# Kernel optimization log

Hardware: AMD Instinct MI355X
Metric: run time of the kernel (lower is better)

Reference implementation:

```python
import jax, jax.numpy as jnp
import numpy as np

BN_EPS = 1e-5


def cond_conv(x, att_w, att_b, weight, pad):
    """CondConv: per-sample expert-mixed conv.
    x: [N,C,H,W]; att_w: [K,C]; att_b: [K]; weight: [K,O,I,kh,kw]; pad: (ph,pw)."""
    pooled = x.mean(axis=(2, 3))                         # [N,C]  (AdaptiveAvgPool2d(1))
    att = jax.nn.sigmoid(pooled @ att_w.T + att_b)       # [N,K]  (1x1 conv + sigmoid)
    agg_w = jnp.einsum('nk,koihw->noihw', att, weight)   # per-sample kernels [N,O,I,kh,kw]

    def conv1(xi, wi):
        return jax.lax.conv_general_dilated(
            xi[None], wi, window_strides=(1, 1),
            padding=[(pad[0], pad[0]), (pad[1], pad[1])],
            dimension_numbers=('NCHW', 'OIHW', 'NCHW'))[0]

    return jax.vmap(conv1)(x, agg_w)                     # [N,O,H,W]


def batchnorm(x, gamma, beta):
    # training-mode BN: biased batch stats over (N,H,W)
    mean = x.mean(axis=(0, 2, 3), keepdims=True)
    var = x.var(axis=(0, 2, 3), keepdims=True)
    xn = (x - mean) * jax.lax.rsqrt(var + BN_EPS)
    return xn * gamma[None, :, None, None] + beta[None, :, None, None]


def channel_shuffle(x, g):
    N, C, H, W = x.shape
    return x.reshape(N, g, C // g, H, W).transpose(0, 2, 1, 3, 4).reshape(N, C, H, W)


def setup_inputs() -> dict:
    key = jax.random.key(0)
    ks = jax.random.split(key, 8)
    N, C, H, W = 32, 256, 64, 64
    Cb, K = C // 4, 4
    inp = {
        'x': jax.random.normal(ks[0], (N, C, H, W), jnp.float32),
        'sq_att_w': jax.random.normal(ks[1], (K, Cb), jnp.float32) * 0.1,
        'sq_att_b': jnp.zeros((K,), jnp.float32),
        'sq_w': jax.random.normal(ks[2], (K, Cb, Cb, 3, 3), jnp.float32) * 0.05,
        'sq_g': jnp.ones((Cb,), jnp.float32),
        'sq_b': jnp.zeros((Cb,), jnp.float32),
        'ver_att_w': jax.random.normal(ks[3], (K, Cb), jnp.float32) * 0.1,
        'ver_att_b': jnp.zeros((K,), jnp.float32),
        'ver_w': jax.random.normal(ks[4], (K, Cb, Cb, 3, 1), jnp.float32) * 0.05,
        'ver_g': jnp.ones((Cb,), jnp.float32),
        'ver_b': jnp.zeros((Cb,), jnp.float32),
        'hor_att_w': jax.random.normal(ks[5], (K, Cb), jnp.float32) * 0.1,
        'hor_att_b': jnp.zeros((K,), jnp.float32),
        'hor_w': jax.random.normal(ks[6], (K, Cb, Cb, 1, 3), jnp.float32) * 0.05,
        'hor_g': jnp.ones((Cb,), jnp.float32),
        'hor_b': jnp.zeros((Cb,), jnp.float32),
    }
    return inp


def reference(x, sq_att_w, sq_att_b, sq_w, sq_g, sq_b,
              ver_att_w, ver_att_b, ver_w, ver_g, ver_b,
              hor_att_w, hor_att_b, hor_w, hor_g, hor_b):
    # q_Split: chunk into 4 along channels
    s0, s1, s2, s3 = jnp.split(x, 4, axis=1)
    # square branch: CondConv 3x3 pad 1 + BN
    sq = batchnorm(cond_conv(s1, sq_att_w, sq_att_b, sq_w, (1, 1)), sq_g, sq_b)
    # vertical branch: CondConv 3x1 pad (1,0) + BN (crop layer is Identity since offset=0)
    ve = batchnorm(cond_conv(s2, ver_att_w, ver_att_b, ver_w, (1, 0)), ver_g, ver_b)
    # horizontal branch: CondConv 1x3 pad (0,1) + BN
    ho = batchnorm(cond_conv(s3, hor_att_w, hor_att_b, hor_w, (0, 1)), hor_g, hor_b)
    out = jnp.concatenate((s0, sq, ve, ho), axis=1)
    return channel_shuffle(out, 8)
```

## Files before the change

kernel.cpp:

```cpp
#include <hip/hip_runtime.h>
#include <cstddef>
#include <cstdint>


typedef __attribute__((ext_vector_type(8))) short frag8;
typedef __attribute__((ext_vector_type(16))) float accf16;

#define HW 4096
#define CNT_INV (1.0f / 131072.0f)
#define CSTR 1056
#define RSTR 8448
#define XT_BR (32ull * 66 * 8448)

#define WS_POOLED 0
#define WS_SS     24576
#define WS_PST    24960
#define WS_WBF_SQ  221568
#define WS_WBF_VER 811392
#define WS_WBF_HOR 1008000
#define WS_XT      1204608
#define WS_CVOUT   14586240

__device__ __forceinline__ int shuf_ch(int c) { return ((c & 31) << 3) | (c >> 5); }

__device__ __forceinline__ unsigned bf16pair(float a, float b) {
    unsigned ua = __builtin_bit_cast(unsigned, a);
    unsigned ub = __builtin_bit_cast(unsigned, b);
    ua = (ua + 0x7fffu + ((ua >> 16) & 1u)) >> 16;
    ub = (ub + 0x7fffu + ((ub >> 16) & 1u)) >> 16;
    return ua | (ub << 16);
}

__device__ __forceinline__ unsigned short bf16r(float a) {
    unsigned ua = __builtin_bit_cast(unsigned, a);
    return (unsigned short)((ua + 0x7fffu + ((ua >> 16) & 1u)) >> 16);
}

__device__ __forceinline__ float bf16lo(unsigned u) {
    return __builtin_bit_cast(float, u << 16);
}
__device__ __forceinline__ float bf16hi(unsigned u) {
    return __builtin_bit_cast(float, u & 0xffff0000u);
}

__device__ __forceinline__ void gload_lds16(const void* g, void* l) {
    __builtin_amdgcn_global_load_lds(
        (const __attribute__((address_space(1))) void*)g,
        (__attribute__((address_space(3))) void*)l, 16, 0, 0);
}

__global__ void __launch_bounds__(256) prepass_kernel(
    const float* __restrict__ x, unsigned char* __restrict__ xt,
    float* __restrict__ pooled4) {
    const int bid = blockIdx.x;
    const int hq = bid & 3;
    const int c8 = (bid >> 2) & 7;
    const int n = (bid >> 5) & 31;
    const int b = bid >> 10;
    const int tid = threadIdx.x;
    const int w = tid & 63, q = tid >> 6;
    const float* xb = x + (size_t)(n * 256 + 64 * (b + 1) + c8 * 8) * HW;
    unsigned char* xtb = xt + (size_t)b * XT_BR + (size_t)n * 66 * RSTR + c8 * CSTR;

    float ps[8] = {0.f, 0.f, 0.f, 0.f, 0.f, 0.f, 0.f, 0.f};
#pragma unroll
    for (int it = 0; it < 4; ++it) {
        const int h = hq * 16 + it * 4 + q;
        float v[8];
#pragma unroll
        for (int j = 0; j < 8; ++j) v[j] = xb[(size_t)j * HW + h * 64 + w];
        unsigned pk[4];
#pragma unroll
        for (int j = 0; j < 4; ++j) pk[j] = bf16pair(v[2 * j], v[2 * j + 1]);
        *(uint4*)(xtb + (size_t)(h + 1) * RSTR + (w + 1) * 16) = *(uint4*)pk;
#pragma unroll
        for (int j = 0; j < 8; ++j) ps[j] += v[j];
    }
    if (hq == 0) {
        for (int idx = tid; idx < 260; idx += 256) {
            int p, slot;
            if (idx < 66)       { p = 0;         slot = idx; }
            else if (idx < 132) { p = 65;        slot = idx - 66; }
            else if (idx < 196) { p = idx - 131; slot = 0; }
            else                { p = idx - 195; slot = 65; }
            *(uint4*)(xtb + (size_t)p * RSTR + slot * 16) = uint4{0, 0, 0, 0};
        }
    }
    __shared__ float red[4][8];
#pragma unroll
    for (int j = 0; j < 8; ++j)
#pragma unroll
        for (int off = 32; off; off >>= 1) ps[j] += __shfl_down(ps[j], off, 64);
    if ((tid & 63) == 0)
#pragma unroll
        for (int j = 0; j < 8; ++j) red[q][j] = ps[j];
    __syncthreads();
    if (tid < 8)
        pooled4[hq * 6144 + (b * 32 + n) * 64 + c8 * 8 + tid] =
            red[0][tid] + red[1][tid] + red[2][tid] + red[3][tid];
}

template <int TAPS>
__device__ __forceinline__ void aggbf_body(const float* __restrict__ w,
                                           const float* __restrict__ pooled_b,
                                           const float* __restrict__ aw,
                                           const float* __restrict__ ab,
                                           unsigned* __restrict__ wbf, int bid) {
    const int tid = threadIdx.x;
    int idx = bid * 256 + tid;
    int ip = idx & 31;
    int o  = (idx >> 5) & 63;
    int t  = (idx >> 11) % TAPS;
    int n  = (idx >> 11) / TAPS;

    __shared__ float satt[4];
    if (tid < 64) {
        const int base = n * 64 + tid;
        float p = (pooled_b[base] + pooled_b[base + 6144] +
                   pooled_b[base + 12288] + pooled_b[base + 18432]) *
                  (1.f / 4096.f);
#pragma unroll
        for (int k = 0; k < 4; ++k) {
            float v = p * aw[k * 64 + tid];
#pragma unroll
            for (int off = 32; off; off >>= 1) v += __shfl_down(v, off, 64);
            if (tid == 0) satt[k] = 1.f / (1.f + expf(-(v + ab[k])));
        }
    }
    __syncthreads();
    const float a0 = satt[0], a1 = satt[1], a2 = satt[2], a3 = satt[3];

    constexpr int PS = 64 * 64 * TAPS;
    int base = (o * 64 + ip * 2) * TAPS + t;
    float v0 = a0*w[base] + a1*w[PS+base] + a2*w[2*PS+base] + a3*w[3*PS+base];
    int base1 = base + TAPS;
    float v1 = a0*w[base1] + a1*w[PS+base1] + a2*w[2*PS+base1] + a3*w[3*PS+base1];
    int f = ip >> 2, jj = ip & 3;
    wbf[(((n * TAPS + t) * 8 + f) * 64 + o) * 4 + jj] = bf16pair(v0, v1);
}

__global__ void __launch_bounds__(256) aggbf_all_kernel(
    const float* __restrict__ pooled,
    const float* __restrict__ aw0, const float* __restrict__ ab0,
    const float* __restrict__ aw1, const float* __restrict__ ab1,
    const float* __restrict__ aw2, const float* __restrict__ ab2,
    const float* __restrict__ sq_w, const float* __restrict__ ver_w,
    const float* __restrict__ hor_w,
    unsigned* __restrict__ wsq, unsigned* __restrict__ wver,
    unsigned* __restrict__ whor) {
    int bid = blockIdx.x;
    if (bid < 2304)
        aggbf_body<9>(sq_w, pooled, aw0, ab0, wsq, bid);
    else if (bid < 3072)
        aggbf_body<3>(ver_w, pooled + 2048, aw1, ab1, wver, bid - 2304);
    else
        aggbf_body<3>(hor_w, pooled + 4096, aw2, ab2, whor, bid - 3072);
}

#define LOADA(dst, tt) \
    _Pragma("unroll") for (int kk = 0; kk < 4; ++kk) { \
        dst[kk]     = wp[(tt) * 512 + kk * 128]; \
        dst[4 + kk] = wp[(tt) * 512 + kk * 128 + 32]; \
    }

#define TAPSTEP(tt, CUR) { \
    const int r_ = (tt) / KW, dw_ = (tt) % KW - PW; \
    const unsigned char* bp_ = xs + (rh * 2 + r_) * RSTR + hi * CSTR + \
                               (wcol + dw_ + 1) * 16; \
    _Pragma("unroll") for (int kk = 0; kk < 4; ++kk) { \
        frag8 b0 = *(const frag8*)(bp_ + kk * 2 * CSTR); \
        frag8 b1 = *(const frag8*)(bp_ + kk * 2 * CSTR + RSTR); \
        a00 = __builtin_amdgcn_mfma_f32_32x32x16_bf16(CUR[kk],     b0, a00, 0, 0, 0); \
        a10 = __builtin_amdgcn_mfma_f32_32x32x16_bf16(CUR[4 + kk], b0, a10, 0, 0, 0); \
        a01 = __builtin_amdgcn_mfma_f32_32x32x16_bf16(CUR[kk],     b1, a01, 0, 0, 0); \
        a11 = __builtin_amdgcn_mfma_f32_32x32x16_bf16(CUR[4 + kk], b1, a11, 0, 0, 0); \
    } }

template <int KH, int KW, int PH, int PW>
__device__ __forceinline__ void conv_body(
    const unsigned char* __restrict__ xt, const unsigned* __restrict__ wbf,
    unsigned short* __restrict__ cvout, float* __restrict__ pst, int cbase,
    int bid, unsigned char* xs, float (*red1)[2][2][16],
    float (*red2)[2][2][16]) {
    constexpr int TAPS = KH * KW;
    constexpr int HB = 4;
    constexpr int ROWS = HB + KH - 1;
    constexpr int TOT = ROWS * RSTR;
    constexpr int NCH = (TOT + 1023) >> 10;
    const int hb = bid & 15, n = bid >> 4;
    const int h0 = hb * HB;
    const int tid = threadIdx.x;
    const int lane = tid & 63;
    const int wv = tid >> 6;
    const int rh = wv >> 1, wn = wv & 1;
    const int l31 = lane & 31, hi = lane >> 5;
    const int wcol = wn * 32 + l31;

    {
        const unsigned char* src = xt +
            (size_t)(n * 66 + h0 + (KH == 1 ? 1 : 0)) * RSTR + lane * 16;
#pragma unroll
        for (int c = wv; c < NCH; c += 4)
            gload_lds16(src + (c << 10), xs + (c << 10));
    }

    const frag8* wp = (const frag8*)wbf + (size_t)n * TAPS * 512 + hi * 64 + l31;

    frag8 aA[8], aB[8];
    LOADA(aA, 0);
    __syncthreads();

    accf16 a00 = {}, a01 = {}, a10 = {}, a11 = {};
#pragma unroll
    for (int t = 0; t < TAPS; t += 2) {
        if (t + 1 < TAPS) LOADA(aB, t + 1);
        TAPSTEP(t, aA);
        if (t + 2 < TAPS) LOADA(aA, t + 2);
        if (t + 1 < TAPS) TAPSTEP(t + 1, aB);
    }

    {
        unsigned short* cb = cvout + (size_t)(n * 192 + (cbase - 64)) * HW +
                             (h0 + rh * 2) * 64 + wcol;
#pragma unroll
        for (int rg = 0; rg < 16; ++rg) {
            const int o = (rg & 3) + 8 * (rg >> 2) + 4 * hi;
            unsigned short* p0 = cb + (size_t)o * HW;
            p0[0]  = bf16r(a00[rg]);
            p0[64] = bf16r(a01[rg]);
            unsigned short* p1 = cb + (size_t)(o + 32) * HW;
            p1[0]  = bf16r(a10[rg]);
            p1[64] = bf16r(a11[rg]);
        }
    }

#pragma unroll
    for (int rg = 0; rg < 16; ++rg) {
        float u1 = a00[rg] + a01[rg];
        float u2 = a00[rg] * a00[rg] + a01[rg] * a01[rg];
        float w1 = a10[rg] + a11[rg];
        float w2 = a10[rg] * a10[rg] + a11[rg] * a11[rg];
#pragma unroll
        for (int off = 16; off; off >>= 1) {
            u1 += __shfl_down(u1, off, 32);
            u2 += __shfl_down(u2, off, 32);
            w1 += __shfl_down(w1, off, 32);
            w2 += __shfl_down(w2, off, 32);
        }
        if (l31 == 0) {
            red1[wv][0][hi][rg] = u1; red2[wv][0][hi][rg] = u2;
            red1[wv][1][hi][rg] = w1; red2[wv][1][hi][rg] = w2;
        }
    }
    __syncthreads();
    if (tid < 64) {
        const int rg = tid & 15, hi2 = (tid >> 4) & 1, wm2 = tid >> 5;
        float s1 = 0.f, s2 = 0.f;
#pragma unroll
        for (int v = 0; v < 4; ++v) {
            s1 += red1[v][wm2][hi2][rg];
            s2 += red2[v][wm2][hi2][rg];
        }
        const int o = wm2 * 32 + (rg & 3) + 8 * (rg >> 2) + 4 * hi2;
        const int slot = n * 16 + hb;
        pst[o * 1024 + slot] = s1;
        pst[o * 1024 + 512 + slot] = s2;
    }
}

__device__ __forceinline__ void s0_body(const float* __restrict__ x,
                                        float* __restrict__ out, int sid) {
    const int c8 = sid & 7, n = sid >> 3, tid = threadIdx.x;
#pragma unroll
    for (int j = 0; j < 8; ++j) {
        const int c = c8 * 8 + j;
        const float4* s = (const float4*)(x + (size_t)(n * 256 + c) * HW);
        float4* d = (float4*)(out + (size_t)(n * 256 + shuf_ch(c)) * HW);
#pragma unroll
        for (int it = 0; it < 4; ++it) d[tid + it * 256] = s[tid + it * 256];
    }
}

__global__ void __launch_bounds__(256, 3) conv_all_kernel(
    const float* __restrict__ x, const unsigned char* __restrict__ xt,
    const unsigned* __restrict__ wsq, const unsigned* __restrict__ wver,
    const unsigned* __restrict__ whor,
    unsigned short* __restrict__ cvout, float* __restrict__ pst,
    float* __restrict__ out) {
    __shared__ __align__(16) unsigned char xs[6 * RSTR + 512];
    __shared__ float red1[4][2][2][16], red2[4][2][2][16];
    int raw = blockIdx.x;
    if (raw >= 1536) { s0_body(x, out, raw - 1536); return; }
    int bid = (raw & 7) * 192 + (raw >> 3);
    if (bid < 512)
        conv_body<3, 3, 1, 1>(xt, wsq, cvout, pst, 64, bid, xs, red1, red2);
    else if (bid < 1024)
        conv_body<3, 1, 1, 0>(xt + XT_BR, wver, cvout, pst + 65536, 128,
                              bid - 512, xs, red1, red2);
    else
        conv_body<1, 3, 0, 1>(xt + 2 * XT_BR, whor, cvout, pst + 131072, 192,
                              bid - 1024, xs, red1, red2);
}

__global__ void __launch_bounds__(256) bnstats_all_kernel(
    const float* __restrict__ pst,
    const float* __restrict__ g0, const float* __restrict__ b0,
    const float* __restrict__ g1, const float* __restrict__ b1,
    const float* __restrict__ g2, const float* __restrict__ b2,
    float* __restrict__ ss) {
    int br = blockIdx.x >> 6, o = blockIdx.x & 63, t = threadIdx.x;
    const float* gamma = (br == 0) ? g0 : (br == 1) ? g1 : g2;
    const float* beta  = (br == 0) ? b0 : (br == 1) ? b1 : b2;
    const float* p = pst + br * 65536 + o * 1024;
    float s1 = 0.f, s2 = 0.f;
    for (int i = t; i < 512; i += 256) {
        s1 += p[i];
        s2 += p[512 + i];
    }
#pragma unroll
    for (int off = 32; off; off >>= 1) {
        s1 += __shfl_down(s1, off, 64);
        s2 += __shfl_down(s2, off, 64);
    }
    __shared__ float r1[4], r2[4];
    if ((t & 63) == 0) { r1[t >> 6] = s1; r2[t >> 6] = s2; }
    __syncthreads();
    if (t == 0) {
        float S1 = r1[0] + r1[1] + r1[2] + r1[3];
        float S2 = r2[0] + r2[1] + r2[2] + r2[3];
        float mean = S1 * CNT_INV;
        float var = S2 * CNT_INV - mean * mean;
        float scale = rsqrtf(var + 1e-5f) * gamma[o];
        ss[br * 128 + o * 2 + 0] = scale;
        ss[br * 128 + o * 2 + 1] = beta[o] - mean * scale;
    }
}

__global__ void __launch_bounds__(256) bn_all_kernel(
    const unsigned short* __restrict__ cvout, float* __restrict__ out,
    const float* __restrict__ ss) {
    int g = blockIdx.x;
    int half = g & 1;
    int n = (g >> 1) & 31;
    int o = (g >> 6) & 63;
    int sub = g >> 12;
    float scale = ss[sub * 128 + o * 2], shift = ss[sub * 128 + o * 2 + 1];
    const uint4* src = (const uint4*)(cvout +
        (size_t)(n * 192 + sub * 64 + o) * HW + half * 2048) + threadIdx.x;
    float* dst = out + (size_t)(n * 256 + shuf_ch(64 * (sub + 1) + o)) * HW +
                 half * 2048 + threadIdx.x * 8;
    uint4 r = *src;
    float4 f0, f1;
    f0.x = fmaf(bf16lo(r.x), scale, shift);
    f0.y = fmaf(bf16hi(r.x), scale, shift);
    f0.z = fmaf(bf16lo(r.y), scale, shift);
    f0.w = fmaf(bf16hi(r.y), scale, shift);
    f1.x = fmaf(bf16lo(r.z), scale, shift);
    f1.y = fmaf(bf16hi(r.z), scale, shift);
    f1.z = fmaf(bf16lo(r.w), scale, shift);
    f1.w = fmaf(bf16hi(r.w), scale, shift);
    *(float4*)dst = f0;
    *(float4*)(dst + 4) = f1;
}

extern "C" void kernel_launch(void* const* d_in, const int* in_sizes, int n_in,
                              void* d_out, int out_size, void* d_ws, size_t ws_size,
                              hipStream_t stream) {
    const float* x        = (const float*)d_in[0];
    const float* sq_att_w = (const float*)d_in[1];
    const float* sq_att_b = (const float*)d_in[2];
    const float* sq_w     = (const float*)d_in[3];
    const float* sq_g     = (const float*)d_in[4];
    const float* sq_b     = (const float*)d_in[5];
    const float* ver_att_w= (const float*)d_in[6];
    const float* ver_att_b= (const float*)d_in[7];
    const float* ver_w    = (const float*)d_in[8];
    const float* ver_g    = (const float*)d_in[9];
    const float* ver_b    = (const float*)d_in[10];
    const float* hor_att_w= (const float*)d_in[11];
    const float* hor_att_b= (const float*)d_in[12];
    const float* hor_w    = (const float*)d_in[13];
    const float* hor_g    = (const float*)d_in[14];
    const float* hor_b    = (const float*)d_in[15];
    float* out = (float*)d_out;
    float* ws = (float*)d_ws;

    float* pooled = ws + WS_POOLED;
    float* ss     = ws + WS_SS;
    float* pst    = ws + WS_PST;
    unsigned* wbf_sq  = (unsigned*)(ws + WS_WBF_SQ);
    unsigned* wbf_ver = (unsigned*)(ws + WS_WBF_VER);
    unsigned* wbf_hor = (unsigned*)(ws + WS_WBF_HOR);
    unsigned char* xt = (unsigned char*)(ws + WS_XT);
    unsigned short* cvout = (unsigned short*)(ws + WS_CVOUT);

    prepass_kernel<<<3072, 256, 0, stream>>>(x, xt, pooled);
    aggbf_all_kernel<<<3840, 256, 0, stream>>>(pooled,
                                               sq_att_w, sq_att_b,
                                               ver_att_w, ver_att_b,
                                               hor_att_w, hor_att_b,
                                               sq_w, ver_w, hor_w,
                                               wbf_sq, wbf_ver, wbf_hor);
    conv_all_kernel<<<1792, 256, 0, stream>>>(x, xt, wbf_sq, wbf_ver, wbf_hor,
                                              cvout, pst, out);
    bnstats_all_kernel<<<192, 256, 0, stream>>>(pst, sq_g, sq_b, ver_g, ver_b,
                                                hor_g, hor_b, ss);
    bn_all_kernel<<<12288, 256, 0, stream>>>(cvout, out, ss);
}
```

Measured before the change: 144.0 us.

## Fuse conv, BN stats and BN apply into one cooperative persistent kernel

Replaces the conv, BN-stats and BN-apply launches with a single cooperative kernel of 512 blocks. Each block computes all three branch tiles for one (n, hb) pair and keeps the results packed as bf16 in registers. It then uses two grid syncs: one to reduce the BN statistics, one to broadcast scale and shift before writing the final output. This avoids the bf16 conv output round trip through global memory and two kernel launches. In exchange each block does three convs in sequence at lower occupancy (launch bounds 2), adds grid-sync costs, and keeps the old path as a fallback if the cooperative launch fails.

```diff
diff --git a/kernel.cpp b/kernel.cpp
--- a/kernel.cpp
+++ b/kernel.cpp
@@ -1,4 +1,5 @@
 #include <hip/hip_runtime.h>
+#include <hip/hip_cooperative_groups.h>
 #include <cstddef>
 #include <cstdint>
 
@@ -29,11 +30,6 @@
     ua = (ua + 0x7fffu + ((ua >> 16) & 1u)) >> 16;
     ub = (ub + 0x7fffu + ((ub >> 16) & 1u)) >> 16;
     return ua | (ub << 16);
-}
-
-__device__ __forceinline__ unsigned short bf16r(float a) {
-    unsigned ua = __builtin_bit_cast(unsigned, a);
-    return (unsigned short)((ua + 0x7fffu + ((ua >> 16) & 1u)) >> 16);
 }
 
 __device__ __forceinline__ float bf16lo(unsigned u) {
@@ -69,10 +65,10 @@
         float v[8];
 #pragma unroll
         for (int j = 0; j < 8; ++j) v[j] = xb[(size_t)j * HW + h * 64 + w];
-        unsigned pk[4];
-#pragma unroll
-        for (int j = 0; j < 4; ++j) pk[j] = bf16pair(v[2 * j], v[2 * j + 1]);
-        *(uint4*)(xtb + (size_t)(h + 1) * RSTR + (w + 1) * 16) = *(uint4*)pk;
+        unsigned pkk[4];
+#pragma unroll
+        for (int j = 0; j < 4; ++j) pkk[j] = bf16pair(v[2 * j], v[2 * j + 1]);
+        *(uint4*)(xtb + (size_t)(h + 1) * RSTR + (w + 1) * 16) = *(uint4*)pkk;
 #pragma unroll
         for (int j = 0; j < 8; ++j) ps[j] += v[j];
     }
@@ -177,21 +173,16 @@
     } }
 
 template <int KH, int KW, int PH, int PW>
-__device__ __forceinline__ void conv_body(
+__device__ __forceinline__ void conv_tile(
     const unsigned char* __restrict__ xt, const unsigned* __restrict__ wbf,
-    unsigned short* __restrict__ cvout, float* __restrict__ pst, int cbase,
-    int bid, unsigned char* xs, float (*red1)[2][2][16],
-    float (*red2)[2][2][16]) {
+    float* __restrict__ pst, int n, int hb, unsigned char* xs,
+    float (*red1)[2][2][16], float (*red2)[2][2][16], unsigned (&pk)[16][2]) {
     constexpr int TAPS = KH * KW;
-    constexpr int HB = 4;
-    constexpr int ROWS = HB + KH - 1;
-    constexpr int TOT = ROWS * RSTR;
-    constexpr int NCH = (TOT + 1023) >> 10;
-    const int hb = bid & 15, n = bid >> 4;
-    const int h0 = hb * HB;
+    constexpr int ROWS = 4 + KH - 1;
+    constexpr int NCH = (ROWS * RSTR + 1023) >> 10;
+    const int h0 = hb * 4;
     const int tid = threadIdx.x;
-    const int lane = tid & 63;
-    const int wv = tid >> 6;
+    const int lane = tid & 63, wv = tid >> 6;
     const int rh = wv >> 1, wn = wv & 1;
     const int l31 = lane & 31, hi = lane >> 5;
     const int wcol = wn * 32 + l31;
@@ -205,7 +196,6 @@
     }
 
     const frag8* wp = (const frag8*)wbf + (size_t)n * TAPS * 512 + hi * 64 + l31;
-
     frag8 aA[8], aB[8];
     LOADA(aA, 0);
     __syncthreads();
@@ -219,19 +209,10 @@
         if (t + 1 < TAPS) TAPSTEP(t + 1, aB);
     }
 
-    {
-        unsigned short* cb = cvout + (size_t)(n * 192 + (cbase - 64)) * HW +
-                             (h0 + rh * 2) * 64 + wcol;
-#pragma unroll
-        for (int rg = 0; rg < 16; ++rg) {
-            const int o = (rg & 3) + 8 * (rg >> 2) + 4 * hi;
-            unsigned short* p0 = cb + (size_t)o * HW;
-            p0[0]  = bf16r(a00[rg]);
-            p0[64] = bf16r(a01[rg]);
-            unsigned short* p1 = cb + (size_t)(o + 32) * HW;
-            p1[0]  = bf16r(a10[rg]);
-            p1[64] = bf16r(a11[rg]);
-        }
+#pragma unroll
+    for (int rg = 0; rg < 16; ++rg) {
+        pk[rg][0] = bf16pair(a00[rg], a01[rg]);
+        pk[rg][1] = bf16pair(a10[rg], a11[rg]);
     }
 
 #pragma unroll
@@ -281,7 +262,121 @@
     }
 }
 
-__global__ void __launch_bounds__(256, 3) conv_all_kernel(
+__device__ __forceinline__ void write_tile(
+    float* __restrict__ out, const float* __restrict__ lss, int br, int cbase,
+    int n, int hb, const unsigned (&pk)[16][2], int rh, int wn, int hi, int l31) {
+    const int wcol = wn * 32 + l31;
+    float* ob = out + (size_t)n * 256 * HW + (hb * 4 + rh * 2) * 64 + wcol;
+#pragma unroll
+    for (int rg = 0; rg < 16; ++rg) {
+        const int o = (rg & 3) + 8 * (rg >> 2) + 4 * hi;
+        {
+            float sc = lss[br * 128 + o * 2], sh = lss[br * 128 + o * 2 + 1];
+            float* p = ob + (size_t)shuf_ch(cbase + o) * HW;
+            p[0]  = fmaf(bf16lo(pk[rg][0]), sc, sh);
+            p[64] = fmaf(bf16hi(pk[rg][0]), sc, sh);
+        }
+        {
+            float sc = lss[br * 128 + (o + 32) * 2];
+            float sh = lss[br * 128 + (o + 32) * 2 + 1];
+            float* p = ob + (size_t)shuf_ch(cbase + 32 + o) * HW;
+            p[0]  = fmaf(bf16lo(pk[rg][1]), sc, sh);
+            p[64] = fmaf(bf16hi(pk[rg][1]), sc, sh);
+        }
+    }
+}
+
+__global__ void __launch_bounds__(256, 2) coop_kernel(
+    const float* __restrict__ x, const unsigned char* __restrict__ xt,
+    const unsigned* __restrict__ wsq, const unsigned* __restrict__ wver,
+    const unsigned* __restrict__ whor, float* __restrict__ pst,
+    float* __restrict__ ss, float* __restrict__ out,
+    const float* __restrict__ g0, const float* __restrict__ b0,
+    const float* __restrict__ g1, const float* __restrict__ b1,
+    const float* __restrict__ g2, const float* __restrict__ b2) {
+    __shared__ __align__(16) unsigned char xs[6 * RSTR + 512];
+    __shared__ float red1[4][2][2][16], red2[4][2][2][16];
+    __shared__ float rr1[4], rr2[4];
+    const int bid = blockIdx.x;
+    const int sbid = (bid & 7) * 64 + (bid >> 3);
+    const int n = sbid >> 4, hb = sbid & 15;
+    const int tid = threadIdx.x;
+    const int lane = tid & 63, wv = tid >> 6;
+    const int rh = wv >> 1, wn = wv & 1, l31 = lane & 31, hi = lane >> 5;
+
+    unsigned pk0[16][2], pk1[16][2], pk2[16][2];
+    conv_tile<3, 3, 1, 1>(xt, wsq, pst, n, hb, xs, red1, red2, pk0);
+    conv_tile<3, 1, 1, 0>(xt + XT_BR, wver, pst + 65536, n, hb, xs, red1, red2, pk1);
+    conv_tile<1, 3, 0, 1>(xt + 2 * XT_BR, whor, pst + 131072, n, hb, xs, red1, red2, pk2);
+    if ((bid & 1) == 0) s0_body(x, out, bid >> 1);
+
+    __threadfence();
+    cooperative_groups::this_grid().sync();
+
+    if (bid < 192) {
+        const int br = bid >> 6, o = bid & 63;
+        const float* gm = (br == 0) ? g0 : (br == 1) ? g1 : g2;
+        const float* bt = (br == 0) ? b0 : (br == 1) ? b1 : b2;
+        const float* p = pst + br * 65536 + o * 1024;
+        float s1 = 0.f, s2 = 0.f;
+        for (int i = tid; i < 512; i += 256) { s1 += p[i]; s2 += p[512 + i]; }
+#pragma unroll
+        for (int off = 32; off; off >>= 1) {
+            s1 += __shfl_down(s1, off, 64);
+            s2 += __shfl_down(s2, off, 64);
+        }
+        if ((tid & 63) == 0) { rr1[tid >> 6] = s1; rr2[tid >> 6] = s2; }
+        __syncthreads();
+        if (tid == 0) {
+            float S1 = rr1[0] + rr1[1] + rr1[2] + rr1[3];
+            float S2 = rr2[0] + rr2[1] + rr2[2] + rr2[3];
+            float mean = S1 * CNT_INV;
+            float var = S2 * CNT_INV - mean * mean;
+            float sc = rsqrtf(var + 1e-5f) * gm[o];
+            ss[br * 128 + o * 2] = sc;
+            ss[br * 128 + o * 2 + 1] = bt[o] - mean * sc;
+        }
+    }
+    __threadfence();
+    cooperative_groups::this_grid().sync();
+
+    float* lss = (float*)xs;
+    for (int i = tid; i < 384; i += 256) lss[i] = ss[i];
+    __syncthreads();
+
+    write_tile(out, lss, 0, 64, n, hb, pk0, rh, wn, hi, l31);
+    write_tile(out, lss, 1, 128, n, hb, pk1, rh, wn, hi, l31);
+    write_tile(out, lss, 2, 192, n, hb, pk2, rh, wn, hi, l31);
+}
+
+template <int KH, int KW, int PH, int PW>
+__device__ __forceinline__ void conv_fb_body(
+    const unsigned char* __restrict__ xt, const unsigned* __restrict__ wbf,
+    unsigned short* __restrict__ cvout, float* __restrict__ pst, int cbase,
+    int bid2, unsigned char* xs, float (*red1)[2][2][16],
+    float (*red2)[2][2][16]) {
+    const int hb = bid2 & 15, n = bid2 >> 4;
+    unsigned pk[16][2];
+    conv_tile<KH, KW, PH, PW>(xt, wbf, pst, n, hb, xs, red1, red2, pk);
+    const int tid = threadIdx.x;
+    const int lane = tid & 63, wv = tid >> 6;
+    const int rh = wv >> 1, wn = wv & 1, l31 = lane & 31, hi = lane >> 5;
+    const int wcol = wn * 32 + l31;
+    unsigned short* cb = cvout + (size_t)(n * 192 + (cbase - 64)) * HW +
+                         (hb * 4 + rh * 2) * 64 + wcol;
+#pragma unroll
+    for (int rg = 0; rg < 16; ++rg) {
+        const int o = (rg & 3) + 8 * (rg >> 2) + 4 * hi;
+        unsigned short* p0 = cb + (size_t)o * HW;
+        p0[0]  = (unsigned short)(pk[rg][0] & 0xffffu);
+        p0[64] = (unsigned short)(pk[rg][0] >> 16);
+        unsigned short* p1 = cb + (size_t)(o + 32) * HW;
+        p1[0]  = (unsigned short)(pk[rg][1] & 0xffffu);
+        p1[64] = (unsigned short)(pk[rg][1] >> 16);
+    }
+}
+
+__global__ void __launch_bounds__(256, 3) conv_all_fb(
     const float* __restrict__ x, const unsigned char* __restrict__ xt,
     const unsigned* __restrict__ wsq, const unsigned* __restrict__ wver,
     const unsigned* __restrict__ whor,
@@ -293,13 +388,13 @@
     if (raw >= 1536) { s0_body(x, out, raw - 1536); return; }
     int bid = (raw & 7) * 192 + (raw >> 3);
     if (bid < 512)
-        conv_body<3, 3, 1, 1>(xt, wsq, cvout, pst, 64, bid, xs, red1, red2);
+        conv_fb_body<3, 3, 1, 1>(xt, wsq, cvout, pst, 64, bid, xs, red1, red2);
     else if (bid < 1024)
-        conv_body<3, 1, 1, 0>(xt + XT_BR, wver, cvout, pst + 65536, 128,
-                              bid - 512, xs, red1, red2);
+        conv_fb_body<3, 1, 1, 0>(xt + XT_BR, wver, cvout, pst + 65536, 128,
+                                 bid - 512, xs, red1, red2);
     else
-        conv_body<1, 3, 0, 1>(xt + 2 * XT_BR, whor, cvout, pst + 131072, 192,
-                              bid - 1024, xs, red1, red2);
+        conv_fb_body<1, 3, 0, 1>(xt + 2 * XT_BR, whor, cvout, pst + 131072, 192,
+                                 bid - 1024, xs, red1, red2);
 }
 
 __global__ void __launch_bounds__(256) bnstats_all_kernel(
@@ -401,9 +496,23 @@
                                                hor_att_w, hor_att_b,
                                                sq_w, ver_w, hor_w,
                                                wbf_sq, wbf_ver, wbf_hor);
-    conv_all_kernel<<<1792, 256, 0, stream>>>(x, xt, wbf_sq, wbf_ver, wbf_hor,
+
+    const unsigned char* xt_c = xt;
+    const unsigned* wsq_c = wbf_sq;
+    const unsigned* wver_c = wbf_ver;
+    const unsigned* whor_c = wbf_hor;
+    void* args[] = {(void*)&x, (void*)&xt_c, (void*)&wsq_c, (void*)&wver_c,
+                    (void*)&whor_c, (void*)&pst, (void*)&ss, (void*)&out,
+                    (void*)&sq_g, (void*)&sq_b, (void*)&ver_g, (void*)&ver_b,
+                    (void*)&hor_g, (void*)&hor_b};
+    hipError_t e = hipLaunchCooperativeKernel((void*)coop_kernel, dim3(512),
+                                              dim3(256), args, 0, stream);
+    if (e != hipSuccess) {
+        conv_all_fb<<<1792, 256, 0, stream>>>(x, xt, wbf_sq, wbf_ver, wbf_hor,
                                               cvout, pst, out);
-    bnstats_all_kernel<<<192, 256, 0, stream>>>(pst, sq_g, sq_b, ver_g, ver_b,
-                                                hor_g, hor_b, ss);
-    bn_all_kernel<<<12288, 256, 0, stream>>>(cvout, out, ss);
-}
+        bnstats_all_kernel<<<192, 256, 0, stream>>>(pst, sq_g, sq_b,
+                                                    ver_g, ver_b,
+                                                    hor_g, hor_b, ss);
+        bn_all_kernel<<<12288, 256, 0, stream>>>(cvout, out, ss);
+    }
+}
```

Measured after the change: 376.0 us. +161.1%, slower.

## Halve conv row tile for more blocks and fold BN stats into apply kernel

Applied to the files above, without the earlier changes.

The conv kernel now computes 2 output rows per block instead of 4. Each wave holds two accumulators instead of four, which doubles the block count, lowers register and LDS use, and raises launch bounds occupancy to 4 blocks per SM. The separate bnstats kernel is removed, and each BN-apply block now re-reduces the per-channel partial sums itself, which saves one launch. In exchange, halo rows are reloaded more often, and the 12288 apply blocks each redundantly read 2048 partial-stat floats.

```diff
diff --git a/kernel.cpp b/kernel.cpp
--- a/kernel.cpp
+++ b/kernel.cpp
@@ -13,13 +13,12 @@
 #define XT_BR (32ull * 66 * 8448)
 
 #define WS_POOLED 0
-#define WS_SS     24576
-#define WS_PST    24960
-#define WS_WBF_SQ  221568
-#define WS_WBF_VER 811392
-#define WS_WBF_HOR 1008000
-#define WS_XT      1204608
-#define WS_CVOUT   14586240
+#define WS_PST    24576
+#define WS_WBF_SQ  417792
+#define WS_WBF_VER 1007616
+#define WS_WBF_HOR 1204224
+#define WS_XT      1400832
+#define WS_CVOUT   14782464
 
 __device__ __forceinline__ int shuf_ch(int c) { return ((c & 31) << 3) | (c >> 5); }
 
@@ -69,10 +68,10 @@
         float v[8];
 #pragma unroll
         for (int j = 0; j < 8; ++j) v[j] = xb[(size_t)j * HW + h * 64 + w];
-        unsigned pk[4];
-#pragma unroll
-        for (int j = 0; j < 4; ++j) pk[j] = bf16pair(v[2 * j], v[2 * j + 1]);
-        *(uint4*)(xtb + (size_t)(h + 1) * RSTR + (w + 1) * 16) = *(uint4*)pk;
+        unsigned pkk[4];
+#pragma unroll
+        for (int j = 0; j < 4; ++j) pkk[j] = bf16pair(v[2 * j], v[2 * j + 1]);
+        *(uint4*)(xtb + (size_t)(h + 1) * RSTR + (w + 1) * 16) = *(uint4*)pkk;
 #pragma unroll
         for (int j = 0; j < 8; ++j) ps[j] += v[j];
     }
@@ -165,15 +164,12 @@
 
 #define TAPSTEP(tt, CUR) { \
     const int r_ = (tt) / KW, dw_ = (tt) % KW - PW; \
-    const unsigned char* bp_ = xs + (rh * 2 + r_) * RSTR + hi * CSTR + \
+    const unsigned char* bp_ = xs + (rh + r_) * RSTR + hi * CSTR + \
                                (wcol + dw_ + 1) * 16; \
     _Pragma("unroll") for (int kk = 0; kk < 4; ++kk) { \
         frag8 b0 = *(const frag8*)(bp_ + kk * 2 * CSTR); \
-        frag8 b1 = *(const frag8*)(bp_ + kk * 2 * CSTR + RSTR); \
         a00 = __builtin_amdgcn_mfma_f32_32x32x16_bf16(CUR[kk],     b0, a00, 0, 0, 0); \
         a10 = __builtin_amdgcn_mfma_f32_32x32x16_bf16(CUR[4 + kk], b0, a10, 0, 0, 0); \
-        a01 = __builtin_amdgcn_mfma_f32_32x32x16_bf16(CUR[kk],     b1, a01, 0, 0, 0); \
-        a11 = __builtin_amdgcn_mfma_f32_32x32x16_bf16(CUR[4 + kk], b1, a11, 0, 0, 0); \
     } }
 
 template <int KH, int KW, int PH, int PW>
@@ -183,15 +179,12 @@
     int bid, unsigned char* xs, float (*red1)[2][2][16],
     float (*red2)[2][2][16]) {
     constexpr int TAPS = KH * KW;
-    constexpr int HB = 4;
-    constexpr int ROWS = HB + KH - 1;
-    constexpr int TOT = ROWS * RSTR;
-    constexpr int NCH = (TOT + 1023) >> 10;
-    const int hb = bid & 15, n = bid >> 4;
-    const int h0 = hb * HB;
+    constexpr int ROWS = 2 + KH - 1;
+    constexpr int NCH = (ROWS * RSTR + 1023) >> 10;
+    const int hb = bid & 31, n = bid >> 5;
+    const int h0 = hb * 2;
     const int tid = threadIdx.x;
-    const int lane = tid & 63;
-    const int wv = tid >> 6;
+    const int lane = tid & 63, wv = tid >> 6;
     const int rh = wv >> 1, wn = wv & 1;
     const int l31 = lane & 31, hi = lane >> 5;
     const int wcol = wn * 32 + l31;
@@ -205,12 +198,11 @@
     }
 
     const frag8* wp = (const frag8*)wbf + (size_t)n * TAPS * 512 + hi * 64 + l31;
-
     frag8 aA[8], aB[8];
     LOADA(aA, 0);
     __syncthreads();
 
-    accf16 a00 = {}, a01 = {}, a10 = {}, a11 = {};
+    accf16 a00 = {}, a10 = {};
 #pragma unroll
     for (int t = 0; t < TAPS; t += 2) {
         if (t + 1 < TAPS) LOADA(aB, t + 1);
@@ -221,25 +213,19 @@
 
     {
         unsigned short* cb = cvout + (size_t)(n * 192 + (cbase - 64)) * HW +
-                             (h0 + rh * 2) * 64 + wcol;
+                             (h0 + rh) * 64 + wcol;
 #pragma unroll
         for (int rg = 0; rg < 16; ++rg) {
             const int o = (rg & 3) + 8 * (rg >> 2) + 4 * hi;
-            unsigned short* p0 = cb + (size_t)o * HW;
-            p0[0]  = bf16r(a00[rg]);
-            p0[64] = bf16r(a01[rg]);
-            unsigned short* p1 = cb + (size_t)(o + 32) * HW;
-            p1[0]  = bf16r(a10[rg]);
-            p1[64] = bf16r(a11[rg]);
+            cb[(size_t)o * HW]        = bf16r(a00[rg]);
+            cb[(size_t)(o + 32) * HW] = bf16r(a10[rg]);
         }
     }
 
 #pragma unroll
     for (int rg = 0; rg < 16; ++rg) {
-        float u1 = a00[rg] + a01[rg];
-        float u2 = a00[rg] * a00[rg] + a01[rg] * a01[rg];
-        float w1 = a10[rg] + a11[rg];
-        float w2 = a10[rg] * a10[rg] + a11[rg] * a11[rg];
+        float u1 = a00[rg], u2 = a00[rg] * a00[rg];
+        float w1 = a10[rg], w2 = a10[rg] * a10[rg];
 #pragma unroll
         for (int off = 16; off; off >>= 1) {
             u1 += __shfl_down(u1, off, 32);
@@ -262,9 +248,9 @@
             s2 += red2[v][wm2][hi2][rg];
         }
         const int o = wm2 * 32 + (rg & 3) + 8 * (rg >> 2) + 4 * hi2;
-        const int slot = n * 16 + hb;
-        pst[o * 1024 + slot] = s1;
-        pst[o * 1024 + 512 + slot] = s2;
+        const int slot = n * 32 + hb;
+        pst[o * 2048 + slot] = s1;
+        pst[o * 2048 + 1024 + slot] = s2;
     }
 }
 
@@ -281,74 +267,70 @@
     }
 }
 
-__global__ void __launch_bounds__(256, 3) conv_all_kernel(
+__global__ void __launch_bounds__(256, 4) conv_all_kernel(
     const float* __restrict__ x, const unsigned char* __restrict__ xt,
     const unsigned* __restrict__ wsq, const unsigned* __restrict__ wver,
     const unsigned* __restrict__ whor,
     unsigned short* __restrict__ cvout, float* __restrict__ pst,
     float* __restrict__ out) {
-    __shared__ __align__(16) unsigned char xs[6 * RSTR + 512];
+    __shared__ __align__(16) unsigned char xs[4 * RSTR + 512];
     __shared__ float red1[4][2][2][16], red2[4][2][2][16];
     int raw = blockIdx.x;
-    if (raw >= 1536) { s0_body(x, out, raw - 1536); return; }
-    int bid = (raw & 7) * 192 + (raw >> 3);
-    if (bid < 512)
+    if (raw >= 3072) { s0_body(x, out, raw - 3072); return; }
+    int bid = (raw & 7) * 384 + (raw >> 3);
+    if (bid < 1024)
         conv_body<3, 3, 1, 1>(xt, wsq, cvout, pst, 64, bid, xs, red1, red2);
-    else if (bid < 1024)
-        conv_body<3, 1, 1, 0>(xt + XT_BR, wver, cvout, pst + 65536, 128,
-                              bid - 512, xs, red1, red2);
+    else if (bid < 2048)
+        conv_body<3, 1, 1, 0>(xt + XT_BR, wver, cvout, pst + 131072, 128,
+                              bid - 1024, xs, red1, red2);
     else
-        conv_body<1, 3, 0, 1>(xt + 2 * XT_BR, whor, cvout, pst + 131072, 192,
-                              bid - 1024, xs, red1, red2);
-}
-
-__global__ void __launch_bounds__(256) bnstats_all_kernel(
+        conv_body<1, 3, 0, 1>(xt + 2 * XT_BR, whor, cvout, pst + 262144, 192,
+                              bid - 2048, xs, red1, red2);
+}
+
+__global__ void __launch_bounds__(256) bn_all_kernel(
+    const unsigned short* __restrict__ cvout, float* __restrict__ out,
     const float* __restrict__ pst,
     const float* __restrict__ g0, const float* __restrict__ b0,
     const float* __restrict__ g1, const float* __restrict__ b1,
-    const float* __restrict__ g2, const float* __restrict__ b2,
-    float* __restrict__ ss) {
-    int br = blockIdx.x >> 6, o = blockIdx.x & 63, t = threadIdx.x;
-    const float* gamma = (br == 0) ? g0 : (br == 1) ? g1 : g2;
-    const float* beta  = (br == 0) ? b0 : (br == 1) ? b1 : b2;
-    const float* p = pst + br * 65536 + o * 1024;
-    float s1 = 0.f, s2 = 0.f;
-    for (int i = t; i < 512; i += 256) {
-        s1 += p[i];
-        s2 += p[512 + i];
-    }
-#pragma unroll
-    for (int off = 32; off; off >>= 1) {
-        s1 += __shfl_down(s1, off, 64);
-        s2 += __shfl_down(s2, off, 64);
-    }
-    __shared__ float r1[4], r2[4];
-    if ((t & 63) == 0) { r1[t >> 6] = s1; r2[t >> 6] = s2; }
-    __syncthreads();
-    if (t == 0) {
-        float S1 = r1[0] + r1[1] + r1[2] + r1[3];
-        float S2 = r2[0] + r2[1] + r2[2] + r2[3];
-        float mean = S1 * CNT_INV;
-        float var = S2 * CNT_INV - mean * mean;
-        float scale = rsqrtf(var + 1e-5f) * gamma[o];
-        ss[br * 128 + o * 2 + 0] = scale;
-        ss[br * 128 + o * 2 + 1] = beta[o] - mean * scale;
-    }
-}
-
-__global__ void __launch_bounds__(256) bn_all_kernel(
-    const unsigned short* __restrict__ cvout, float* __restrict__ out,
-    const float* __restrict__ ss) {
+    const float* __restrict__ g2, const float* __restrict__ b2) {
     int g = blockIdx.x;
     int half = g & 1;
     int n = (g >> 1) & 31;
     int o = (g >> 6) & 63;
     int sub = g >> 12;
-    float scale = ss[sub * 128 + o * 2], shift = ss[sub * 128 + o * 2 + 1];
+    const int t = threadIdx.x;
+
+    const float* p = pst + sub * 131072 + o * 2048;
+    float s1 = 0.f, s2 = 0.f;
+#pragma unroll
+    for (int i = t; i < 1024; i += 256) { s1 += p[i]; s2 += p[1024 + i]; }
+#pragma unroll
+    for (int off = 32; off; off >>= 1) {
+        s1 += __shfl_down(s1, off, 64);
+        s2 += __shfl_down(s2, off, 64);
+    }
+    __shared__ float r1[4], r2[4], sc_sh[2];
+    if ((t & 63) == 0) { r1[t >> 6] = s1; r2[t >> 6] = s2; }
+    __syncthreads();
+    if (t == 0) {
+        const float* gm = (sub == 0) ? g0 : (sub == 1) ? g1 : g2;
+        const float* bt = (sub == 0) ? b0 : (sub == 1) ? b1 : b2;
+        float S1 = r1[0] + r1[1] + r1[2] + r1[3];
+        float S2 = r2[0] + r2[1] + r2[2] + r2[3];
+        float mean = S1 * CNT_INV;
+        float var = S2 * CNT_INV - mean * mean;
+        float sc = rsqrtf(var + 1e-5f) * gm[o];
+        sc_sh[0] = sc;
+        sc_sh[1] = bt[o] - mean * sc;
+    }
+    __syncthreads();
+    const float scale = sc_sh[0], shift = sc_sh[1];
+
     const uint4* src = (const uint4*)(cvout +
-        (size_t)(n * 192 + sub * 64 + o) * HW + half * 2048) + threadIdx.x;
+        (size_t)(n * 192 + sub * 64 + o) * HW + half * 2048) + t;
     float* dst = out + (size_t)(n * 256 + shuf_ch(64 * (sub + 1) + o)) * HW +
-                 half * 2048 + threadIdx.x * 8;
+                 half * 2048 + t * 8;
     uint4 r = *src;
     float4 f0, f1;
     f0.x = fmaf(bf16lo(r.x), scale, shift);
@@ -386,7 +368,6 @@
     float* ws = (float*)d_ws;
 
     float* pooled = ws + WS_POOLED;
-    float* ss     = ws + WS_SS;
     float* pst    = ws + WS_PST;
     unsigned* wbf_sq  = (unsigned*)(ws + WS_WBF_SQ);
     unsigned* wbf_ver = (unsigned*)(ws + WS_WBF_VER);
@@ -401,9 +382,9 @@
                                                hor_att_w, hor_att_b,
                                                sq_w, ver_w, hor_w,
                                                wbf_sq, wbf_ver, wbf_hor);
-    conv_all_kernel<<<1792, 256, 0, stream>>>(x, xt, wbf_sq, wbf_ver, wbf_hor,
+    conv_all_kernel<<<3328, 256, 0, stream>>>(x, xt, wbf_sq, wbf_ver, wbf_hor,
                                               cvout, pst, out);
-    bnstats_all_kernel<<<192, 256, 0, stream>>>(pst, sq_g, sq_b, ver_g, ver_b,
-                                                hor_g, hor_b, ss);
-    bn_all_kernel<<<12288, 256, 0, stream>>>(cvout, out, ss);
-}
+    bn_all_kernel<<<12288, 256, 0, stream>>>(cvout, out, pst,
+                                             sq_g, sq_b, ver_g, ver_b,
+                                             hor_g, hor_b);
+}
```

Result: slower. 166.2 us (+15.4%).

## Remap conv wave tiling: each wave owns 32 out-channels across all 4 rows

Applied to the files above, without the earlier changes.

Changes how the four waves split the 64-channel by 4-row by 64-column output tile. Before, each wave computed 64 channels by 2 rows. Now each wave computes 32 channels by 4 rows. Per tap, each wave loads half as many weight fragments from global memory and twice as many activation fragments from LDS. This cuts register pressure for weights and global weight traffic, at the cost of more LDS reads, and the BN partial-stat reduction is simplified to match.

```diff
diff --git a/kernel.cpp b/kernel.cpp
--- a/kernel.cpp
+++ b/kernel.cpp
@@ -69,10 +69,10 @@
         float v[8];
 #pragma unroll
         for (int j = 0; j < 8; ++j) v[j] = xb[(size_t)j * HW + h * 64 + w];
-        unsigned pk[4];
-#pragma unroll
-        for (int j = 0; j < 4; ++j) pk[j] = bf16pair(v[2 * j], v[2 * j + 1]);
-        *(uint4*)(xtb + (size_t)(h + 1) * RSTR + (w + 1) * 16) = *(uint4*)pk;
+        unsigned pkk[4];
+#pragma unroll
+        for (int j = 0; j < 4; ++j) pkk[j] = bf16pair(v[2 * j], v[2 * j + 1]);
+        *(uint4*)(xtb + (size_t)(h + 1) * RSTR + (w + 1) * 16) = *(uint4*)pkk;
 #pragma unroll
         for (int j = 0; j < 8; ++j) ps[j] += v[j];
     }
@@ -158,41 +158,40 @@
 }
 
 #define LOADA(dst, tt) \
-    _Pragma("unroll") for (int kk = 0; kk < 4; ++kk) { \
-        dst[kk]     = wp[(tt) * 512 + kk * 128]; \
-        dst[4 + kk] = wp[(tt) * 512 + kk * 128 + 32]; \
-    }
+    _Pragma("unroll") for (int kk = 0; kk < 4; ++kk) \
+        dst[kk] = wp[(tt) * 512 + kk * 128];
 
 #define TAPSTEP(tt, CUR) { \
     const int r_ = (tt) / KW, dw_ = (tt) % KW - PW; \
-    const unsigned char* bp_ = xs + (rh * 2 + r_) * RSTR + hi * CSTR + \
+    const unsigned char* bp_ = xs + r_ * RSTR + hi * CSTR + \
                                (wcol + dw_ + 1) * 16; \
     _Pragma("unroll") for (int kk = 0; kk < 4; ++kk) { \
-        frag8 b0 = *(const frag8*)(bp_ + kk * 2 * CSTR); \
-        frag8 b1 = *(const frag8*)(bp_ + kk * 2 * CSTR + RSTR); \
-        a00 = __builtin_amdgcn_mfma_f32_32x32x16_bf16(CUR[kk],     b0, a00, 0, 0, 0); \
-        a10 = __builtin_amdgcn_mfma_f32_32x32x16_bf16(CUR[4 + kk], b0, a10, 0, 0, 0); \
-        a01 = __builtin_amdgcn_mfma_f32_32x32x16_bf16(CUR[kk],     b1, a01, 0, 0, 0); \
-        a11 = __builtin_amdgcn_mfma_f32_32x32x16_bf16(CUR[4 + kk], b1, a11, 0, 0, 0); \
+        const unsigned char* q_ = bp_ + kk * 2 * CSTR; \
+        frag8 b0 = *(const frag8*)(q_); \
+        frag8 b1 = *(const frag8*)(q_ + RSTR); \
+        frag8 b2 = *(const frag8*)(q_ + 2 * RSTR); \
+        frag8 b3 = *(const frag8*)(q_ + 3 * RSTR); \
+        ac0 = __builtin_amdgcn_mfma_f32_32x32x16_bf16(CUR[kk], b0, ac0, 0, 0, 0); \
+        ac1 = __builtin_amdgcn_mfma_f32_32x32x16_bf16(CUR[kk], b1, ac1, 0, 0, 0); \
+        ac2 = __builtin_amdgcn_mfma_f32_32x32x16_bf16(CUR[kk], b2, ac2, 0, 0, 0); \
+        ac3 = __builtin_amdgcn_mfma_f32_32x32x16_bf16(CUR[kk], b3, ac3, 0, 0, 0); \
     } }
 
 template <int KH, int KW, int PH, int PW>
 __device__ __forceinline__ void conv_body(
     const unsigned char* __restrict__ xt, const unsigned* __restrict__ wbf,
     unsigned short* __restrict__ cvout, float* __restrict__ pst, int cbase,
-    int bid, unsigned char* xs, float (*red1)[2][2][16],
-    float (*red2)[2][2][16]) {
+    int bid, unsigned char* xs, float (*red1)[2][16],
+    float (*red2)[2][16]) {
     constexpr int TAPS = KH * KW;
     constexpr int HB = 4;
     constexpr int ROWS = HB + KH - 1;
-    constexpr int TOT = ROWS * RSTR;
-    constexpr int NCH = (TOT + 1023) >> 10;
+    constexpr int NCH = (ROWS * RSTR + 1023) >> 10;
     const int hb = bid & 15, n = bid >> 4;
     const int h0 = hb * HB;
     const int tid = threadIdx.x;
-    const int lane = tid & 63;
-    const int wv = tid >> 6;
-    const int rh = wv >> 1, wn = wv & 1;
+    const int lane = tid & 63, wv = tid >> 6;
+    const int wm = wv >> 1, wn = wv & 1;
     const int l31 = lane & 31, hi = lane >> 5;
     const int wcol = wn * 32 + l31;
 
@@ -204,13 +203,13 @@
             gload_lds16(src + (c << 10), xs + (c << 10));
     }
 
-    const frag8* wp = (const frag8*)wbf + (size_t)n * TAPS * 512 + hi * 64 + l31;
-
-    frag8 aA[8], aB[8];
+    const frag8* wp = (const frag8*)wbf + (size_t)n * TAPS * 512 +
+                      hi * 64 + wm * 32 + l31;
+    frag8 aA[4], aB[4];
     LOADA(aA, 0);
     __syncthreads();
 
-    accf16 a00 = {}, a01 = {}, a10 = {}, a11 = {};
+    accf16 ac0 = {}, ac1 = {}, ac2 = {}, ac3 = {};
 #pragma unroll
     for (int t = 0; t < TAPS; t += 2) {
         if (t + 1 < TAPS) LOADA(aB, t + 1);
@@ -221,46 +220,35 @@
 
     {
         unsigned short* cb = cvout + (size_t)(n * 192 + (cbase - 64)) * HW +
-                             (h0 + rh * 2) * 64 + wcol;
+                             h0 * 64 + wcol;
 #pragma unroll
         for (int rg = 0; rg < 16; ++rg) {
-            const int o = (rg & 3) + 8 * (rg >> 2) + 4 * hi;
-            unsigned short* p0 = cb + (size_t)o * HW;
-            p0[0]  = bf16r(a00[rg]);
-            p0[64] = bf16r(a01[rg]);
-            unsigned short* p1 = cb + (size_t)(o + 32) * HW;
-            p1[0]  = bf16r(a10[rg]);
-            p1[64] = bf16r(a11[rg]);
+            const int o = wm * 32 + (rg & 3) + 8 * (rg >> 2) + 4 * hi;
+            unsigned short* p = cb + (size_t)o * HW;
+            p[0]   = bf16r(ac0[rg]);
+            p[64]  = bf16r(ac1[rg]);
+            p[128] = bf16r(ac2[rg]);
+            p[192] = bf16r(ac3[rg]);
         }
     }
 
 #pragma unroll
     for (int rg = 0; rg < 16; ++rg) {
-        float u1 = a00[rg] + a01[rg];
-        float u2 = a00[rg] * a00[rg] + a01[rg] * a01[rg];
-        float w1 = a10[rg] + a11[rg];
-        float w2 = a10[rg] * a10[rg] + a11[rg] * a11[rg];
+        float u1 = (ac0[rg] + ac1[rg]) + (ac2[rg] + ac3[rg]);
+        float u2 = (ac0[rg] * ac0[rg] + ac1[rg] * ac1[rg]) +
+                   (ac2[rg] * ac2[rg] + ac3[rg] * ac3[rg]);
 #pragma unroll
         for (int off = 16; off; off >>= 1) {
             u1 += __shfl_down(u1, off, 32);
             u2 += __shfl_down(u2, off, 32);
-            w1 += __shfl_down(w1, off, 32);
-            w2 += __shfl_down(w2, off, 32);
         }
-        if (l31 == 0) {
-            red1[wv][0][hi][rg] = u1; red2[wv][0][hi][rg] = u2;
-            red1[wv][1][hi][rg] = w1; red2[wv][1][hi][rg] = w2;
-        }
+        if (l31 == 0) { red1[wv][hi][rg] = u1; red2[wv][hi][rg] = u2; }
     }
     __syncthreads();
     if (tid < 64) {
         const int rg = tid & 15, hi2 = (tid >> 4) & 1, wm2 = tid >> 5;
-        float s1 = 0.f, s2 = 0.f;
-#pragma unroll
-        for (int v = 0; v < 4; ++v) {
-            s1 += red1[v][wm2][hi2][rg];
-            s2 += red2[v][wm2][hi2][rg];
-        }
+        float s1 = red1[wm2 * 2][hi2][rg] + red1[wm2 * 2 + 1][hi2][rg];
+        float s2 = red2[wm2 * 2][hi2][rg] + red2[wm2 * 2 + 1][hi2][rg];
         const int o = wm2 * 32 + (rg & 3) + 8 * (rg >> 2) + 4 * hi2;
         const int slot = n * 16 + hb;
         pst[o * 1024 + slot] = s1;
@@ -288,7 +276,7 @@
     unsigned short* __restrict__ cvout, float* __restrict__ pst,
     float* __restrict__ out) {
     __shared__ __align__(16) unsigned char xs[6 * RSTR + 512];
-    __shared__ float red1[4][2][2][16], red2[4][2][2][16];
+    __shared__ float red1[4][2][16], red2[4][2][16];
     int raw = blockIdx.x;
     if (raw >= 1536) { s0_body(x, out, raw - 1536); return; }
     int bid = (raw & 7) * 192 + (raw >> 3);
```

Result: slower. 179.6 us (+24.7%).
